# Kernel tuning notes

Hardware: AMD Instinct MI355X
Metric: run time of the kernel (lower is better)

The kernel has to match this reference:

```python
import jax, jax.numpy as jnp
import numpy as np
import math

B, C, H, W = 32, 1024, 32, 32
D = 1024  # d == in_channels == H*W (required by the module's own code)


def _conv1x1(x, w, b):
    # x: (B,C,H,W), w: (out,in), b: (out,)
    return jnp.einsum('bchw,dc->bdhw', x, w) + b[None, :, None, None]


def setup_inputs() -> dict:
    key = jax.random.key(0)
    ks = jax.random.split(key, 20)
    s = 0.02
    d = {'x': jax.random.normal(ks[0], (B, C, H, W), dtype=jnp.float32)}
    names = ['w1', 'w2', 'w3', 'w4', 'w5', 'w6', 'w7']
    for i, n in enumerate(names):
        d[n] = s * jax.random.normal(ks[1 + 2 * i], (D, D), dtype=jnp.float32)
        d['b' + n[1:]] = s * jax.random.normal(ks[2 + 2 * i], (D,), dtype=jnp.float32)
    d['wl'] = s * jax.random.normal(ks[16], (D, D), dtype=jnp.float32)
    d['bl'] = s * jax.random.normal(ks[17], (D,), dtype=jnp.float32)
    return d


def reference(x, w1, b1, w2, b2, w3, b3, w4, b4, w5, b5, w6, b6, w7, b7, wl, bl):
    b, c, h, w = x.shape
    d = w1.shape[0]
    n = h * w
    scale = 1.0 / math.sqrt(d)

    def lin(z):  # Linear(d,d) over the LAST dim (= n = d here)
        return jnp.einsum('bdn,mn->bdm', z, wl) + bl

    # --- attention block 1 ---
    Q1 = _conv1x1(x, w1, b1).reshape(b, d, n)
    K1 = _conv1x1(x, w2, b2).reshape(b, d, n)
    V1 = _conv1x1(x, w3, b3).reshape(b, d, n)
    A1 = jax.nn.softmax(jnp.einsum('bdn,bdm->bnm', Q1, K1) * scale, axis=-1)  # (b,n,n)
    O1 = jnp.einsum('bdm,bnm->bdn', V1, A1)  # V1 @ A1^T -> (b,d,n)
    X1 = O1.reshape(b, d, h, w) + x

    # --- attention block 2 ---
    Q2 = lin(_conv1x1(X1, w5, b5).reshape(b, d, n))
    K2 = lin(_conv1x1(X1, w6, b6).reshape(b, d, n))
    V2 = lin(_conv1x1(X1, w7, b7).reshape(b, d, n))
    A2 = jax.nn.softmax(jnp.einsum('bdn,bdm->bnm', Q2, K2) * scale, axis=-1)  # (b,n,n)
    O2 = jnp.einsum('bnm,bkm->bkn', A2, V2)  # (A2 @ V2^T)^T -> (b,d,n)
    X2 = _conv1x1(O2.reshape(b, d, h, w), w4, b4) + X1
    return X2
```

## Files before the change

kernel.cpp:

```cpp
#include <hip/hip_runtime.h>
#include <hip/hip_bf16.h>
#include <cstdint>

typedef unsigned short u16;
typedef __bf16 bf16x8 __attribute__((ext_vector_type(8)));
typedef float f32x4 __attribute__((ext_vector_type(4)));
typedef unsigned short us8 __attribute__((ext_vector_type(8)));

#define AS1 __attribute__((address_space(1)))
#define AS3 __attribute__((address_space(3)))

__device__ __forceinline__ float b2f(u16 u) {
    union { float f; uint32_t i; } c; c.i = ((uint32_t)u) << 16; return c.f;
}
__device__ __forceinline__ u16 f2b(float f) {
    union { float f; uint32_t i; } c; c.f = f;
    return (u16)((c.i + 0x7fffu + ((c.i >> 16) & 1u)) >> 16);
}

#define BM 256
#define BN 256
#define BK 64
#define GK 1024
#define GN 1024
#define NKT (GK / BK)

#define BAR asm volatile("s_barrier" ::: "memory")

template <typename OutT>
__global__ __launch_bounds__(512, 2) void gemm_nt(
    const u16* __restrict__ A, long long sA,
    const u16* __restrict__ B, long long sB,
    OutT* __restrict__ C, long long sC,
    const float* __restrict__ bias, int biasMode,
    const u16* __restrict__ res, long long sR,
    float scale)
{
    __shared__ __align__(16) char smem[131072];

    const int t = threadIdx.x;
    const int orig = blockIdx.x;
    const int id2 = (orig & 7) * 64 + (orig >> 3);
    const int bz = id2 >> 4;
    const int by = (id2 >> 2) & 3;
    const int bx = id2 & 3;

    const u16* Ab = A + (size_t)bz * sA + (size_t)(by * BM) * GK;
    const u16* Bb = B + (size_t)bz * sB + (size_t)(bx * BN) * GK;

    const int wave = t >> 6, lane = t & 63;
    const int l16 = lane & 15, quad = lane >> 4;
    const int wr = wave >> 2;
    const int wc = wave & 3;
    const int bq = l16 & 7;

    f32x4 acc[8][4] = {};

    int geoff[2], ldoff[2];
    #pragma unroll
    for (int i = 0; i < 2; ++i) {
        const int c = t + 512 * i;
        const int r = c >> 3, js = c & 7;
        geoff[i] = r * GK + (js ^ (r & 7)) * 8;
        ldoff[i] = c * 16;
    }

    #define STG_A(tile, h)                                                               \
        _Pragma("unroll")                                                                \
        for (int i = 0; i < 2; ++i)                                                      \
            __builtin_amdgcn_global_load_lds(                                            \
                (AS1 const void*)(Ab + (size_t)(h) * 128 * GK + geoff[i] + (tile) * BK), \
                (AS3 void*)(smem + ((tile) & 1) * 65536 + (h) * 16384 + ldoff[i]),       \
                16, 0, 0);
    #define STG_B(tile, h)                                                               \
        _Pragma("unroll")                                                                \
        for (int i = 0; i < 2; ++i)                                                      \
            __builtin_amdgcn_global_load_lds(                                            \
                (AS1 const void*)(Bb + (size_t)(h) * 128 * GK + geoff[i] + (tile) * BK), \
                (AS3 void*)(smem + ((tile) & 1) * 65536 + 32768 + (h) * 16384 + ldoff[i]), \
                16, 0, 0);

    auto ldsA = [&](int p, int mh, int mi, int kk) -> const bf16x8* {
        return (const bf16x8*)(smem + p * 65536 + wr * 16384
            + (mh * 64 + mi * 16 + l16) * 128 + (((kk * 4 + quad) ^ bq) * 16));
    };
    auto ldsB = [&](int p, int nh, int ni, int kk) -> const bf16x8* {
        return (const bf16x8*)(smem + p * 65536 + 32768 + (wc >> 1) * 16384
            + ((wc & 1) * 64 + nh * 32 + ni * 16 + l16) * 128 + (((kk * 4 + quad) ^ bq) * 16));
    };

    auto group = [&](int tile) {
        const int p = tile & 1;
        const bool stA = (tile + 1) < NKT;
        const bool stB = (tile + 2) < NKT;
        bf16x8 af[4][2], b0[2][2], b1[2][2];

        #pragma unroll
        for (int mi = 0; mi < 4; ++mi)
            #pragma unroll
            for (int kk = 0; kk < 2; ++kk)
                af[mi][kk] = *ldsA(p, 0, mi, kk);
        #pragma unroll
        for (int ni = 0; ni < 2; ++ni)
            #pragma unroll
            for (int kk = 0; kk < 2; ++kk)
                b0[ni][kk] = *ldsB(p, 0, ni, kk);
        if (stA) { STG_A(tile + 1, 0) }
        BAR;
        __builtin_amdgcn_s_setprio(1);
        #pragma unroll
        for (int kk = 0; kk < 2; ++kk)
            #pragma unroll
            for (int mi = 0; mi < 4; ++mi)
                #pragma unroll
                for (int ni = 0; ni < 2; ++ni)
                    acc[mi][ni] = __builtin_amdgcn_mfma_f32_16x16x32_bf16(af[mi][kk], b0[ni][kk], acc[mi][ni], 0, 0, 0);
        __builtin_amdgcn_s_setprio(0);
        BAR;

        #pragma unroll
        for (int ni = 0; ni < 2; ++ni)
            #pragma unroll
            for (int kk = 0; kk < 2; ++kk)
                b1[ni][kk] = *ldsB(p, 1, ni, kk);
        if (stA) { STG_A(tile + 1, 1) }
        BAR;
        __builtin_amdgcn_s_setprio(1);
        #pragma unroll
        for (int kk = 0; kk < 2; ++kk)
            #pragma unroll
            for (int mi = 0; mi < 4; ++mi)
                #pragma unroll
                for (int ni = 0; ni < 2; ++ni)
                    acc[mi][2 + ni] = __builtin_amdgcn_mfma_f32_16x16x32_bf16(af[mi][kk], b1[ni][kk], acc[mi][2 + ni], 0, 0, 0);
        __builtin_amdgcn_s_setprio(0);
        BAR;

        #pragma unroll
        for (int mi = 0; mi < 4; ++mi)
            #pragma unroll
            for (int kk = 0; kk < 2; ++kk)
                af[mi][kk] = *ldsA(p, 1, mi, kk);
        if (stB) { STG_B(tile + 2, 0) }
        BAR;
        __builtin_amdgcn_s_setprio(1);
        #pragma unroll
        for (int kk = 0; kk < 2; ++kk)
            #pragma unroll
            for (int mi = 0; mi < 4; ++mi)
                #pragma unroll
                for (int ni = 0; ni < 2; ++ni)
                    acc[4 + mi][2 + ni] = __builtin_amdgcn_mfma_f32_16x16x32_bf16(af[mi][kk], b1[ni][kk], acc[4 + mi][2 + ni], 0, 0, 0);
        __builtin_amdgcn_s_setprio(0);
        BAR;

        if (stB) { STG_B(tile + 2, 1) }
        BAR;
        __builtin_amdgcn_s_setprio(1);
        #pragma unroll
        for (int kk = 0; kk < 2; ++kk)
            #pragma unroll
            for (int mi = 0; mi < 4; ++mi)
                #pragma unroll
                for (int ni = 0; ni < 2; ++ni)
                    acc[4 + mi][ni] = __builtin_amdgcn_mfma_f32_16x16x32_bf16(af[mi][kk], b0[ni][kk], acc[4 + mi][ni], 0, 0, 0);
        __builtin_amdgcn_s_setprio(0);
        if (stB) { asm volatile("s_waitcnt vmcnt(4)" ::: "memory"); }
        else     { asm volatile("s_waitcnt vmcnt(0)" ::: "memory"); }
        BAR;
    };

    STG_A(0, 0) STG_A(0, 1) STG_B(0, 0) STG_B(0, 1) STG_B(1, 0) STG_B(1, 1)
    asm volatile("s_waitcnt vmcnt(4)" ::: "memory");
    BAR;

    #pragma unroll 1
    for (int j = 0; j < NKT / 2; ++j) {
        group(2 * j);
        group(2 * j + 1);
    }

    float* Cs = (float*)smem;
    #pragma unroll
    for (int mh = 0; mh < 2; ++mh) {
        __syncthreads();
        if (wr == mh) {
            #pragma unroll
            for (int mi = 0; mi < 8; ++mi)
                #pragma unroll
                for (int ni = 0; ni < 4; ++ni) {
                    const int col = wc * 64 + ni * 16 + l16;
                    const int jc = col >> 2, cw = col & 3;
                    #pragma unroll
                    for (int r2 = 0; r2 < 4; ++r2) {
                        const int row = mi * 16 + quad * 4 + r2;
                        Cs[row * 256 + ((jc ^ (row & 15)) << 2) + cw] = acc[mi][ni][r2];
                    }
                }
        }
        __syncthreads();

        if constexpr (__is_same(OutT, u16)) {
            #pragma unroll
            for (int i = 0; i < 8; ++i) {
                const int c = t + 512 * i;
                const int lr = c >> 5, cc = c & 31;
                const int sxy = lr & 15;
                const float* s0 = Cs + lr * 256 + (((cc * 2) ^ sxy) << 2);
                const float* s1 = Cs + lr * 256 + (((cc * 2 + 1) ^ sxy) << 2);
                float4 a = *(const float4*)s0;
                float4 b = *(const float4*)s1;
                const int grow = by * BM + mh * 128 + lr;
                const int gcol = bx * BN + cc * 8;
                const float br = (biasMode == 1) ? bias[grow] : 0.0f;
                float v[8] = {a.x, a.y, a.z, a.w, b.x, b.y, b.z, b.w};
                #pragma unroll
                for (int jj = 0; jj < 8; ++jj) v[jj] = v[jj] * scale + br;
                if (biasMode == 2) {
                    float4 c1 = *(const float4*)(bias + gcol);
                    float4 c2 = *(const float4*)(bias + gcol + 4);
                    v[0] += c1.x; v[1] += c1.y; v[2] += c1.z; v[3] += c1.w;
                    v[4] += c2.x; v[5] += c2.y; v[6] += c2.z; v[7] += c2.w;
                }
                if (res) {
                    us8 rv = *(const us8*)(res + (size_t)bz * sR + (size_t)grow * GN + gcol);
                    #pragma unroll
                    for (int jj = 0; jj < 8; ++jj) v[jj] += b2f(rv[jj]);
                }
                us8 o;
                #pragma unroll
                for (int jj = 0; jj < 8; ++jj) o[jj] = f2b(v[jj]);
                *(us8*)((u16*)C + (size_t)bz * sC + (size_t)grow * GN + gcol) = o;
            }
        } else {
            #pragma unroll
            for (int i = 0; i < 16; ++i) {
                const int c = t + 512 * i;
                const int lr = c >> 6, cc4 = c & 63;
                const float* src = Cs + lr * 256 + ((cc4 ^ (lr & 15)) << 2);
                float4 a = *(const float4*)src;
                const int grow = by * BM + mh * 128 + lr;
                const int gcol = bx * BN + cc4 * 4;
                const float br = (biasMode == 1) ? bias[grow] : 0.0f;
                float v[4] = {a.x, a.y, a.z, a.w};
                #pragma unroll
                for (int jj = 0; jj < 4; ++jj) v[jj] = v[jj] * scale + br;
                if (biasMode == 2) {
                    float4 c1 = *(const float4*)(bias + gcol);
                    v[0] += c1.x; v[1] += c1.y; v[2] += c1.z; v[3] += c1.w;
                }
                if (res) {
                    ushort4 rv = *(const ushort4*)(res + (size_t)bz * sR + (size_t)grow * GN + gcol);
                    v[0] += b2f(rv.x); v[1] += b2f(rv.y); v[2] += b2f(rv.z); v[3] += b2f(rv.w);
                }
                float4 o = {v[0], v[1], v[2], v[3]};
                *(float4*)((float*)C + (size_t)bz * sC + (size_t)grow * GN + gcol) = o;
            }
        }
    }
    #undef STG_A
    #undef STG_B
}

__global__ __launch_bounds__(256) void softmax_rows(u16* __restrict__ S)
{
    const size_t row = blockIdx.x;
    u16* p = S + row * 1024;
    const int t = threadIdx.x;
    ushort4 u = ((const ushort4*)p)[t];
    float v0 = b2f(u.x), v1 = b2f(u.y), v2 = b2f(u.z), v3 = b2f(u.w);

    float m = fmaxf(fmaxf(v0, v1), fmaxf(v2, v3));
    #pragma unroll
    for (int o = 32; o > 0; o >>= 1) m = fmaxf(m, __shfl_xor(m, o, 64));
    __shared__ float red[8];
    const int wave = t >> 6, lane = t & 63;
    if (lane == 0) red[wave] = m;
    __syncthreads();
    m = fmaxf(fmaxf(red[0], red[1]), fmaxf(red[2], red[3]));

    v0 = __expf(v0 - m); v1 = __expf(v1 - m); v2 = __expf(v2 - m); v3 = __expf(v3 - m);
    float s = v0 + v1 + v2 + v3;
    #pragma unroll
    for (int o = 32; o > 0; o >>= 1) s += __shfl_xor(s, o, 64);
    if (lane == 0) red[4 + wave] = s;
    __syncthreads();
    s = red[4] + red[5] + red[6] + red[7];
    const float inv = 1.0f / s;

    u.x = f2b(v0 * inv); u.y = f2b(v1 * inv); u.z = f2b(v2 * inv); u.w = f2b(v3 * inv);
    ((ushort4*)p)[t] = u;
}

__global__ __launch_bounds__(256) void transpose_k(const u16* __restrict__ in, u16* __restrict__ out)
{
    __shared__ u16 tile[64][65];
    const size_t base = (size_t)blockIdx.z * 1024 * 1024;
    const u16* ib = in + base;
    u16* ob = out + base;
    const int t = threadIdx.x;
    const int vc = t & 15;
    const int rr0 = t >> 4;
    const int tr = blockIdx.y * 64, tc = blockIdx.x * 64;

    #pragma unroll
    for (int rr = 0; rr < 4; ++rr) {
        const int row = rr * 16 + rr0;
        ushort4 u = *(const ushort4*)(ib + (size_t)(tr + row) * 1024 + tc + vc * 4);
        tile[row][vc * 4 + 0] = u.x; tile[row][vc * 4 + 1] = u.y;
        tile[row][vc * 4 + 2] = u.z; tile[row][vc * 4 + 3] = u.w;
    }
    __syncthreads();
    #pragma unroll
    for (int rr = 0; rr < 4; ++rr) {
        const int orow = rr * 16 + rr0;
        ushort4 u;
        u.x = tile[vc * 4 + 0][orow]; u.y = tile[vc * 4 + 1][orow];
        u.z = tile[vc * 4 + 2][orow]; u.w = tile[vc * 4 + 3][orow];
        *(ushort4*)(ob + (size_t)(tc + orow) * 1024 + tr + vc * 4) = u;
    }
}

__global__ __launch_bounds__(256) void tconv_k(const float* __restrict__ in, u16* __restrict__ out)
{
    __shared__ float tile[64][65];
    const size_t base = (size_t)blockIdx.z * 1024 * 1024;
    const float* ib = in + base;
    u16* ob = out + base;
    const int t = threadIdx.x;
    const int vc = t & 15;
    const int rr0 = t >> 4;
    const int tr = blockIdx.y * 64, tc = blockIdx.x * 64;

    #pragma unroll
    for (int rr = 0; rr < 4; ++rr) {
        const int row = rr * 16 + rr0;
        float4 u = *(const float4*)(ib + (size_t)(tr + row) * 1024 + tc + vc * 4);
        tile[row][vc * 4 + 0] = u.x; tile[row][vc * 4 + 1] = u.y;
        tile[row][vc * 4 + 2] = u.z; tile[row][vc * 4 + 3] = u.w;
    }
    __syncthreads();
    #pragma unroll
    for (int rr = 0; rr < 4; ++rr) {
        const int orow = rr * 16 + rr0;
        ushort4 u;
        u.x = f2b(tile[vc * 4 + 0][orow]); u.y = f2b(tile[vc * 4 + 1][orow]);
        u.z = f2b(tile[vc * 4 + 2][orow]); u.w = f2b(tile[vc * 4 + 3][orow]);
        *(ushort4*)(ob + (size_t)(tc + orow) * 1024 + tr + vc * 4) = u;
    }
}

struct WPack { const float* in[8]; u16* out[8]; };
__global__ __launch_bounds__(256) void convw_k(WPack p)
{
    const int m = blockIdx.y;
    const int i = (blockIdx.x * 256 + threadIdx.x) * 4;
    float4 v = *(const float4*)(p.in[m] + i);
    ushort4 s;
    s.x = f2b(v.x); s.y = f2b(v.y); s.z = f2b(v.z); s.w = f2b(v.w);
    *(ushort4*)(p.out[m] + i) = s;
}

extern "C" void kernel_launch(void* const* d_in, const int* in_sizes, int n_in,
                              void* d_out, int out_size, void* d_ws, size_t ws_size,
                              hipStream_t stream) {
    const size_t mat = (size_t)32 * 1024 * 1024;
    const long long mm = 1024LL * 1024LL;
    const float sc = 1.0f / 32.0f;

    const float* x  = (const float*)d_in[0];
    const float* w1 = (const float*)d_in[1];  const float* b1 = (const float*)d_in[2];
    const float* w2 = (const float*)d_in[3];  const float* b2 = (const float*)d_in[4];
    const float* w3 = (const float*)d_in[5];  const float* b3 = (const float*)d_in[6];
    const float* w4 = (const float*)d_in[7];  const float* b4 = (const float*)d_in[8];
    const float* w5 = (const float*)d_in[9];  const float* b5 = (const float*)d_in[10];
    const float* w6 = (const float*)d_in[11]; const float* b6 = (const float*)d_in[12];
    const float* w7 = (const float*)d_in[13]; const float* b7 = (const float*)d_in[14];
    const float* wl = (const float*)d_in[15]; const float* bl = (const float*)d_in[16];
    float* out = (float*)d_out;

    u16* A = (u16*)d_ws;
    u16* Bv = A + mat;
    u16* Cv = A + 2 * mat;
    u16* Dv = A + 3 * mat;
    u16* wb = A + 4 * mat;
    u16 *w1b = wb, *w2b = wb + (1<<20), *w3b = wb + 2*(1<<20), *w4b = wb + 3*(1<<20),
        *w5b = wb + 4*(1<<20), *w6b = wb + 5*(1<<20), *w7b = wb + 6*(1<<20), *wlb = wb + 7*(1<<20);
    u16* OutLo = (u16*)d_out;
    u16* OutHi = OutLo + mat;

    WPack wp;
    wp.in[0]=w1; wp.in[1]=w2; wp.in[2]=w3; wp.in[3]=w4; wp.in[4]=w5; wp.in[5]=w6; wp.in[6]=w7; wp.in[7]=wl;
    wp.out[0]=w1b; wp.out[1]=w2b; wp.out[2]=w3b; wp.out[3]=w4b; wp.out[4]=w5b; wp.out[5]=w6b; wp.out[6]=w7b; wp.out[7]=wlb;

    const dim3 blk(256);
    const dim3 blkG(512);
    const dim3 gT(16, 16, 32), gG(512), gS(32 * 1024), gW(1024, 8);

    convw_k<<<gW, blk, 0, stream>>>(wp);
    tconv_k<<<gT, blk, 0, stream>>>(x, A);
    gemm_nt<u16><<<gG, blkG, 0, stream>>>(A, mm, w1b, 0, Bv, mm, b1, 2, nullptr, 0, 1.0f);
    gemm_nt<u16><<<gG, blkG, 0, stream>>>(A, mm, w2b, 0, Cv, mm, b2, 2, nullptr, 0, 1.0f);
    gemm_nt<u16><<<gG, blkG, 0, stream>>>(w3b, 0, A, mm, Dv, mm, b3, 1, nullptr, 0, 1.0f);
    gemm_nt<u16><<<gG, blkG, 0, stream>>>(Bv, mm, Cv, mm, OutLo, mm, nullptr, 0, nullptr, 0, sc);
    softmax_rows<<<gS, blk, 0, stream>>>(OutLo);
    gemm_nt<u16><<<gG, blkG, 0, stream>>>(OutLo, mm, Dv, mm, Bv, mm, nullptr, 0, A, mm, 1.0f);
    transpose_k<<<gT, blk, 0, stream>>>(Bv, A);
    gemm_nt<u16><<<gG, blkG, 0, stream>>>(w5b, 0, Bv, mm, Cv, mm, b5, 1, nullptr, 0, 1.0f);
    gemm_nt<u16><<<gG, blkG, 0, stream>>>(wlb, 0, Cv, mm, Dv, mm, bl, 1, nullptr, 0, 1.0f);
    gemm_nt<u16><<<gG, blkG, 0, stream>>>(w6b, 0, Bv, mm, Cv, mm, b6, 1, nullptr, 0, 1.0f);
    gemm_nt<u16><<<gG, blkG, 0, stream>>>(wlb, 0, Cv, mm, OutLo, mm, bl, 1, nullptr, 0, 1.0f);
    gemm_nt<u16><<<gG, blkG, 0, stream>>>(w7b, 0, Bv, mm, Cv, mm, b7, 1, nullptr, 0, 1.0f);
    gemm_nt<u16><<<gG, blkG, 0, stream>>>(Cv, mm, wlb, 0, OutHi, mm, bl, 2, nullptr, 0, 1.0f);
    gemm_nt<u16><<<gG, blkG, 0, stream>>>(Dv, mm, OutLo, mm, Bv, mm, nullptr, 0, nullptr, 0, sc);
    softmax_rows<<<gS, blk, 0, stream>>>(Bv);
    gemm_nt<u16><<<gG, blkG, 0, stream>>>(Bv, mm, OutHi, mm, Cv, mm, nullptr, 0, nullptr, 0, 1.0f);
    gemm_nt<float><<<gG, blkG, 0, stream>>>(w4b, 0, Cv, mm, out, mm, b4, 1, A, mm, 1.0f);
}
```

Baseline: 1.497 ms.

## Share the Linear-over-n projection across Q2/K2/V2 via matmul reassociation

```diff
diff --git a/kernel.cpp b/kernel.cpp
--- a/kernel.cpp
+++ b/kernel.cpp
@@ -34,7 +34,8 @@
     OutT* __restrict__ C, long long sC,
     const float* __restrict__ bias, int biasMode,
     const u16* __restrict__ res, long long sR,
-    float scale)
+    float scale,
+    const float* __restrict__ r1u, const float* __restrict__ r1v)
 {
     __shared__ __align__(16) char smem[131072];
 
@@ -222,6 +223,13 @@
                     v[0] += c1.x; v[1] += c1.y; v[2] += c1.z; v[3] += c1.w;
                     v[4] += c2.x; v[5] += c2.y; v[6] += c2.z; v[7] += c2.w;
                 }
+                if (r1u) {
+                    const float u = r1u[grow];
+                    float4 c1 = *(const float4*)(r1v + gcol);
+                    float4 c2 = *(const float4*)(r1v + gcol + 4);
+                    v[0] += u * c1.x; v[1] += u * c1.y; v[2] += u * c1.z; v[3] += u * c1.w;
+                    v[4] += u * c2.x; v[5] += u * c2.y; v[6] += u * c2.z; v[7] += u * c2.w;
+                }
                 if (res) {
                     us8 rv = *(const us8*)(res + (size_t)bz * sR + (size_t)grow * GN + gcol);
                     #pragma unroll
@@ -249,6 +257,11 @@
                     float4 c1 = *(const float4*)(bias + gcol);
                     v[0] += c1.x; v[1] += c1.y; v[2] += c1.z; v[3] += c1.w;
                 }
+                if (r1u) {
+                    const float u = r1u[grow];
+                    float4 c1 = *(const float4*)(r1v + gcol);
+                    v[0] += u * c1.x; v[1] += u * c1.y; v[2] += u * c1.z; v[3] += u * c1.w;
+                }
                 if (res) {
                     ushort4 rv = *(const ushort4*)(res + (size_t)bz * sR + (size_t)grow * GN + gcol);
                     v[0] += b2f(rv.x); v[1] += b2f(rv.y); v[2] += b2f(rv.z); v[3] += b2f(rv.w);
@@ -359,6 +372,21 @@
     ushort4 s;
     s.x = f2b(v.x); s.y = f2b(v.y); s.z = f2b(v.z); s.w = f2b(v.w);
     *(ushort4*)(p.out[m] + i) = s;
+}
+
+__global__ __launch_bounds__(256) void rowsum_k(const float* __restrict__ w, float* __restrict__ s)
+{
+    const int m = blockIdx.x;
+    const float* r = w + (size_t)m * 1024;
+    const int t = threadIdx.x;
+    float4 v = ((const float4*)r)[t];
+    float x = v.x + v.y + v.z + v.w;
+    #pragma unroll
+    for (int o = 32; o > 0; o >>= 1) x += __shfl_xor(x, o, 64);
+    __shared__ float red[4];
+    if ((t & 63) == 0) red[t >> 6] = x;
+    __syncthreads();
+    if (t == 0) s[m] = red[0] + red[1] + red[2] + red[3];
 }
 
 extern "C" void kernel_launch(void* const* d_in, const int* in_sizes, int n_in,
@@ -386,6 +414,7 @@
     u16* wb = A + 4 * mat;
     u16 *w1b = wb, *w2b = wb + (1<<20), *w3b = wb + 2*(1<<20), *w4b = wb + 3*(1<<20),
         *w5b = wb + 4*(1<<20), *w6b = wb + 5*(1<<20), *w7b = wb + 6*(1<<20), *wlb = wb + 7*(1<<20);
+    float* swl = (float*)(wb + 8*(1<<20));
     u16* OutLo = (u16*)d_out;
     u16* OutHi = OutLo + mat;
 
@@ -395,25 +424,27 @@
 
     const dim3 blk(256);
     const dim3 blkG(512);
-    const dim3 gT(16, 16, 32), gG(512), gS(32 * 1024), gW(1024, 8);
+    const dim3 gT(16, 16, 32), gG(512), gS(32 * 1024), gW(1024, 8), gR(1024);
+    const float* NUL = nullptr;
 
     convw_k<<<gW, blk, 0, stream>>>(wp);
+    rowsum_k<<<gR, blk, 0, stream>>>(wl, swl);
     tconv_k<<<gT, blk, 0, stream>>>(x, A);
-    gemm_nt<u16><<<gG, blkG, 0, stream>>>(A, mm, w1b, 0, Bv, mm, b1, 2, nullptr, 0, 1.0f);
-    gemm_nt<u16><<<gG, blkG, 0, stream>>>(A, mm, w2b, 0, Cv, mm, b2, 2, nullptr, 0, 1.0f);
-    gemm_nt<u16><<<gG, blkG, 0, stream>>>(w3b, 0, A, mm, Dv, mm, b3, 1, nullptr, 0, 1.0f);
-    gemm_nt<u16><<<gG, blkG, 0, stream>>>(Bv, mm, Cv, mm, OutLo, mm, nullptr, 0, nullptr, 0, sc);
+
+    gemm_nt<u16><<<gG, blkG, 0, stream>>>(A, mm, w1b, 0, Bv, mm, b1, 2, nullptr, 0, 1.0f, NUL, NUL);
+    gemm_nt<u16><<<gG, blkG, 0, stream>>>(A, mm, w2b, 0, Cv, mm, b2, 2, nullptr, 0, 1.0f, NUL, NUL);
+    gemm_nt<u16><<<gG, blkG, 0, stream>>>(w3b, 0, A, mm, Dv, mm, b3, 1, nullptr, 0, 1.0f, NUL, NUL);
+    gemm_nt<u16><<<gG, blkG, 0, stream>>>(Bv, mm, Cv, mm, OutLo, mm, nullptr, 0, nullptr, 0, sc, NUL, NUL);
     softmax_rows<<<gS, blk, 0, stream>>>(OutLo);
-    gemm_nt<u16><<<gG, blkG, 0, stream>>>(OutLo, mm, Dv, mm, Bv, mm, nullptr, 0, A, mm, 1.0f);
+    gemm_nt<u16><<<gG, blkG, 0, stream>>>(OutLo, mm, Dv, mm, Bv, mm, nullptr, 0, A, mm, 1.0f, NUL, NUL);
     transpose_k<<<gT, blk, 0, stream>>>(Bv, A);
-    gemm_nt<u16><<<gG, blkG, 0, stream>>>(w5b, 0, Bv, mm, Cv, mm, b5, 1, nullptr, 0, 1.0f);
-    gemm_nt<u16><<<gG, blkG, 0, stream>>>(wlb, 0, Cv, mm, Dv, mm, bl, 1, nullptr, 0, 1.0f);
-    gemm_nt<u16><<<gG, blkG, 0, stream>>>(w6b, 0, Bv, mm, Cv, mm, b6, 1, nullptr, 0, 1.0f);
-    gemm_nt<u16><<<gG, blkG, 0, stream>>>(wlb, 0, Cv, mm, OutLo, mm, bl, 1, nullptr, 0, 1.0f);
-    gemm_nt<u16><<<gG, blkG, 0, stream>>>(w7b, 0, Bv, mm, Cv, mm, b7, 1, nullptr, 0, 1.0f);
-    gemm_nt<u16><<<gG, blkG, 0, stream>>>(Cv, mm, wlb, 0, OutHi, mm, bl, 2, nullptr, 0, 1.0f);
-    gemm_nt<u16><<<gG, blkG, 0, stream>>>(Dv, mm, OutLo, mm, Bv, mm, nullptr, 0, nullptr, 0, sc);
+
+    gemm_nt<u16><<<gG, blkG, 0, stream>>>(wlb, 0, A, mm, Cv, mm, nullptr, 0, nullptr, 0, 1.0f, NUL, NUL);
+    gemm_nt<u16><<<gG, blkG, 0, stream>>>(Cv, mm, w5b, 0, Dv, mm, bl, 1, nullptr, 0, 1.0f, swl, b5);
+    gemm_nt<u16><<<gG, blkG, 0, stream>>>(Cv, mm, w6b, 0, OutLo, mm, bl, 1, nullptr, 0, 1.0f, swl, b6);
+    gemm_nt<u16><<<gG, blkG, 0, stream>>>(w7b, 0, Cv, mm, OutHi, mm, bl, 2, nullptr, 0, 1.0f, b7, swl);
+    gemm_nt<u16><<<gG, blkG, 0, stream>>>(Dv, mm, OutLo, mm, Bv, mm, nullptr, 0, nullptr, 0, sc, NUL, NUL);
     softmax_rows<<<gS, blk, 0, stream>>>(Bv);
-    gemm_nt<u16><<<gG, blkG, 0, stream>>>(Bv, mm, OutHi, mm, Cv, mm, nullptr, 0, nullptr, 0, 1.0f);
-    gemm_nt<float><<<gG, blkG, 0, stream>>>(w4b, 0, Cv, mm, out, mm, b4, 1, A, mm, 1.0f);
-}
+    gemm_nt<u16><<<gG, blkG, 0, stream>>>(Bv, mm, OutHi, mm, Cv, mm, nullptr, 0, nullptr, 0, 1.0f, NUL, NUL);
+    gemm_nt<float><<<gG, blkG, 0, stream>>>(w4b, 0, Cv, mm, out, mm, b4, 1, A, mm, 1.0f, NUL, NUL);
+}
```

New measurement: 1.348 ms. 1.11x faster.
